# Kernel optimization log

Hardware: AMD Instinct MI355X
Metric: run time of the kernel (lower is better)

The kernel has to match this reference:

```python
import jax, jax.numpy as jnp
import numpy as np

B, H, S = 2, 16, 2048
CTX = 4096


def setup_inputs() -> dict:
    key = jax.random.key(0)
    k1, k2 = jax.random.split(key)
    scores = jax.random.normal(k1, (B, H, S, S), dtype=jnp.float32)
    positions = jnp.arange(CTX, dtype=jnp.float32)  # ALiBi position buffer
    token_indices = jnp.sort(
        jax.random.randint(k2, (B, S), 0, CTX), axis=-1
    ).astype(jnp.int64)
    return {"scores": scores, "positions": positions, "token_indices": token_indices}


def reference(scores, positions, token_indices):
    # scores: [B, H, S, S]; positions: [CTX]; token_indices: [B, S]
    num_heads = scores.shape[1]
    # slopes: 2^(-8*h/H) for h = 1..H
    slopes = jnp.exp2(
        -8.0 * jnp.arange(1, num_heads + 1, dtype=scores.dtype) / num_heads
    )
    pos = positions[token_indices]  # [B, S]
    pos_diff = pos[:, :, None] - pos[:, None, :]  # [B, S, S]
    biases = slopes[None, :, None, None] * pos_diff[:, None, :, :]  # [B, H, S, S]
    return scores - biases
```

## Files before the change

kernel.cpp:

```cpp
#include <hip/hip_runtime.h>


constexpr int B_   = 2;
constexpr int H_   = 16;
constexpr int S_   = 2048;

__global__ void alibi_gather_pos(const float* __restrict__ positions,
                                 const int* __restrict__ token_indices,
                                 float* __restrict__ posg, int n) {
    int t = blockIdx.x * blockDim.x + threadIdx.x;
    if (t < n) {
        posg[t] = positions[token_indices[t]];
    }
}

__global__ __launch_bounds__(256) void alibi_apply(
    const float4* __restrict__ scores4,
    const float* __restrict__ posg,
    float4* __restrict__ out4,
    long n4) {
    const long stride = (long)gridDim.x * blockDim.x;
    for (long idx = (long)blockIdx.x * blockDim.x + threadIdx.x; idx < n4;
         idx += stride) {
        const int  j4  = (int)(idx & (S_ / 4 - 1));
        const long row = idx >> 9;
        const int  i   = (int)(row & (S_ - 1));
        const long bh  = row >> 11;
        const int  h   = (int)(bh & (H_ - 1));
        const int  b   = (int)(bh >> 4);

        const float slope = exp2f(-0.5f * (float)(h + 1));
        const float pi    = posg[b * S_ + i];
        const float4 pj   = *reinterpret_cast<const float4*>(&posg[b * S_ + j4 * 4]);

        const float4 s = scores4[idx];
        float4 o;
        o.x = s.x - slope * (pi - pj.x);
        o.y = s.y - slope * (pi - pj.y);
        o.z = s.z - slope * (pi - pj.z);
        o.w = s.w - slope * (pi - pj.w);
        out4[idx] = o;
    }
}

extern "C" void kernel_launch(void* const* d_in, const int* in_sizes, int n_in,
                              void* d_out, int out_size, void* d_ws, size_t ws_size,
                              hipStream_t stream) {
    const float* scores        = (const float*)d_in[0];
    const float* positions     = (const float*)d_in[1];
    const int*   token_indices = (const int*)d_in[2];

    float* out  = (float*)d_out;
    float* posg = (float*)d_ws;

    const int npos = B_ * S_;
    alibi_gather_pos<<<(npos + 255) / 256, 256, 0, stream>>>(positions,
                                                             token_indices,
                                                             posg, npos);

    const long n4 = (long)B_ * H_ * S_ * (S_ / 4);
    const int  blocks = 2048;
    alibi_apply<<<blocks, 256, 0, stream>>>(
        reinterpret_cast<const float4*>(scores), posg,
        reinterpret_cast<float4*>(out), n4);
}
```

Baseline: 854.9 us.

## Assign row slabs per block, hoist column positions, use nontemporal loads/stores

Replaces the grid-stride flat loop with a fixed mapping where each block handles 32 consecutive rows of one batch-head, each thread covering two float4 columns. Column positions and the slope are loaded once per thread rather than per element, and index arithmetic becomes 32-bit. Scores and outputs use nontemporal loads and stores to avoid polluting caches with streaming data. The fixed mapping relies on compile-time shapes.

```diff
diff --git a/kernel.cpp b/kernel.cpp
--- a/kernel.cpp
+++ b/kernel.cpp
@@ -1,9 +1,14 @@
 #include <hip/hip_runtime.h>
 
 
-constexpr int B_   = 2;
-constexpr int H_   = 16;
-constexpr int S_   = 2048;
+constexpr int B_  = 2;
+constexpr int H_  = 16;
+constexpr int S_  = 2048;
+constexpr int SQ_ = S_ / 4;
+constexpr int ROWS_PER_BLOCK = 32;
+constexpr int BLOCKS_PER_BH  = S_ / ROWS_PER_BLOCK;
+
+typedef float f32x4 __attribute__((ext_vector_type(4)));
 
 __global__ void alibi_gather_pos(const float* __restrict__ positions,
                                  const int* __restrict__ token_indices,
@@ -15,31 +20,46 @@
 }
 
 __global__ __launch_bounds__(256) void alibi_apply(
-    const float4* __restrict__ scores4,
+    const f32x4* __restrict__ scores4,
     const float* __restrict__ posg,
-    float4* __restrict__ out4,
-    long n4) {
-    const long stride = (long)gridDim.x * blockDim.x;
-    for (long idx = (long)blockIdx.x * blockDim.x + threadIdx.x; idx < n4;
-         idx += stride) {
-        const int  j4  = (int)(idx & (S_ / 4 - 1));
-        const long row = idx >> 9;
-        const int  i   = (int)(row & (S_ - 1));
-        const long bh  = row >> 11;
-        const int  h   = (int)(bh & (H_ - 1));
-        const int  b   = (int)(bh >> 4);
+    f32x4* __restrict__ out4) {
+    const int bid  = blockIdx.x;
+    const int bh   = bid >> 6;
+    const int slab = bid & (BLOCKS_PER_BH - 1);
+    const int h    = bh & (H_ - 1);
+    const int b    = bh >> 4;
 
-        const float slope = exp2f(-0.5f * (float)(h + 1));
-        const float pi    = posg[b * S_ + i];
-        const float4 pj   = *reinterpret_cast<const float4*>(&posg[b * S_ + j4 * 4]);
+    const float slope = exp2f(-0.5f * (float)(h + 1));
+    const float* __restrict__ pb = posg + b * S_;
+    const int i0 = slab * ROWS_PER_BLOCK;
 
-        const float4 s = scores4[idx];
-        float4 o;
-        o.x = s.x - slope * (pi - pj.x);
-        o.y = s.y - slope * (pi - pj.y);
-        o.z = s.z - slope * (pi - pj.z);
-        o.w = s.w - slope * (pi - pj.w);
-        out4[idx] = o;
+    const int j4a = threadIdx.x;
+    const int j4b = threadIdx.x + 256;
+    const f32x4 pja = *reinterpret_cast<const f32x4*>(pb + 4 * j4a);
+    const f32x4 pjb = *reinterpret_cast<const f32x4*>(pb + 4 * j4b);
+
+    const int base = (bh * S_ + i0) * SQ_;
+
+    #pragma unroll 4
+    for (int r = 0; r < ROWS_PER_BLOCK; ++r) {
+        const float pi = pb[i0 + r];
+        const int   rb = base + r * SQ_;
+
+        f32x4 s0 = __builtin_nontemporal_load(scores4 + rb + j4a);
+        f32x4 s1 = __builtin_nontemporal_load(scores4 + rb + j4b);
+
+        f32x4 o0, o1;
+        o0.x = s0.x - slope * (pi - pja.x);
+        o0.y = s0.y - slope * (pi - pja.y);
+        o0.z = s0.z - slope * (pi - pja.z);
+        o0.w = s0.w - slope * (pi - pja.w);
+        o1.x = s1.x - slope * (pi - pjb.x);
+        o1.y = s1.y - slope * (pi - pjb.y);
+        o1.z = s1.z - slope * (pi - pjb.z);
+        o1.w = s1.w - slope * (pi - pjb.w);
+
+        __builtin_nontemporal_store(o0, out4 + rb + j4a);
+        __builtin_nontemporal_store(o1, out4 + rb + j4b);
     }
 }
 
@@ -58,9 +78,8 @@
                                                              token_indices,
                                                              posg, npos);
 
-    const long n4 = (long)B_ * H_ * S_ * (S_ / 4);
-    const int  blocks = 2048;
+    const int blocks = B_ * H_ * BLOCKS_PER_BH;
     alibi_apply<<<blocks, 256, 0, stream>>>(
-        reinterpret_cast<const float4*>(scores), posg,
-        reinterpret_cast<float4*>(out), n4);
+        reinterpret_cast<const f32x4*>(scores), posg,
+        reinterpret_cast<f32x4*>(out));
 }
```

Measured after the change: 834.6 us. 2.4% less time.
